# Kernel optimization log

Hardware: AMD Instinct MI355X
Metric: run time of the kernel (lower is better)

The kernel has to match this reference:

```python
import jax, jax.numpy as jnp
import numpy as np


def setup_inputs() -> dict:
    key = jax.random.key(0)
    kx, kf = jax.random.split(key)
    x = jax.random.normal(kx, (4, 8192, 1024), dtype=jnp.float32)
    filt = jax.random.normal(kf, (2048,), dtype=jnp.float32)
    return {"x": x, "filt": filt}


def reference(x, filt):
    # x: (batch, seq, dim); filt: (filter_length,)
    batch, seq, dim = x.shape
    L = filt.shape[0]
    pad = seq + L - 1
    # long-sequence FFT branch (seq > 64)
    xt = jnp.swapaxes(x, 1, 2)                 # (b, d, s)
    fx = jnp.fft.rfft(xt, n=pad, axis=-1)      # (b, d, pad//2+1) complex
    ff = jnp.fft.rfft(filt[::-1], n=pad)       # (pad//2+1,) complex
    conv = jnp.fft.irfft(fx * ff, n=pad, axis=-1)  # (b, d, pad)
    conv = conv[:, :, L - 1:L - 1 + seq]       # valid region, length seq
    return jnp.swapaxes(conv, 1, 2)            # (b, s, d)
```

## Files before the change

kernel.cpp:

```cpp
#include <hip/hip_runtime.h>

typedef unsigned short u16;
typedef unsigned int   u32;

#define BATCH 4
#define SEQ   8192
#define DIM   1024
#define FL    2048
#define TROW  10240

#define BM 512
#define BN 64
#define BK 64
#define NSTAGE 40
#define WOFF 64
#define NW   2272
#define WIN_HI 2174

typedef float  f32x4  __attribute__((ext_vector_type(4)));
typedef __bf16 bf16x8 __attribute__((ext_vector_type(8)));
typedef short  s16x8  __attribute__((ext_vector_type(8)));

typedef const __attribute__((address_space(1))) void* gas_t;
typedef __attribute__((address_space(3))) void* las_t;

__device__ __forceinline__ u16 f2bf(float f) {
  u32 u = __float_as_uint(f);
  u += 0x7fffu + ((u >> 16) & 1u);
  return (u16)(u >> 16);
}

__global__ __launch_bounds__(256) void k_transpose(const float* __restrict__ x,
                                                   u16* __restrict__ xT) {
  __shared__ __align__(16) u16 sm[64 * 66];
  const int bid = blockIdx.x;
  const int tb = bid % (TROW / 64);
  const int db = (bid / (TROW / 64)) % (DIM / 64);
  const int b  = bid / ((TROW / 64) * (DIM / 64));
  const int t0 = tb * 64, d0 = db * 64;
  const int tid = threadIdx.x;

  const int c4 = tid & 15;
  const int lt = tid >> 4;
  const float* xb = x + (size_t)b * SEQ * DIM + d0 + c4 * 4;
  #pragma unroll
  for (int s = 0; s < 64; s += 16) {
    const int tl = lt + s;
    const int t = t0 + tl;
    float4 v = make_float4(0.f, 0.f, 0.f, 0.f);
    if (t < SEQ) v = *(const float4*)(xb + (size_t)t * DIM);
    u32 p0 = (u32)f2bf(v.x) | ((u32)f2bf(v.y) << 16);
    u32 p1 = (u32)f2bf(v.z) | ((u32)f2bf(v.w) << 16);
    u32* dst = (u32*)&sm[tl * 66 + c4 * 4];
    dst[0] = p0;
    dst[1] = p1;
  }
  __syncthreads();
  const int q  = tid & 7;
  const int dl = tid >> 3;
  u16* xo = xT + ((size_t)b * DIM + d0) * TROW + t0 + 8 * q;
  #pragma unroll
  for (int s = 0; s < 2; ++s) {
    const int d = dl + 32 * s;
    u32 w[4];
    #pragma unroll
    for (int h = 0; h < 4; ++h) {
      w[h] = (u32)sm[(8 * q + 2 * h) * 66 + d] |
             ((u32)sm[(8 * q + 2 * h + 1) * 66 + d] << 16);
    }
    *(uint4*)(xo + (size_t)d * TROW) = *(const uint4*)w;
  }
}

__global__ __launch_bounds__(256, 2) void k_conv(const u16* __restrict__ xT,
                                                 const float* __restrict__ filt,
                                                 float* __restrict__ out) {
  __shared__ __align__(16) u16 Wb[NW * 8];
  __shared__ __align__(16) u16 Xs[2][BN * BK];

  const int bid = blockIdx.x;
  const int tb = bid & 15;
  const int db = (bid >> 4) & 15;
  const int b  = bid >> 8;
  const int t0 = tb * BM;
  const int d0 = db * BN;

  const int tid  = threadIdx.x;
  const int wid  = tid >> 6;
  const int lane = tid & 63;
  const int quad = lane >> 4;
  const int lq   = lane & 15;
  const int Tw   = wid * 128;

  for (int w = tid; w < NW; w += 256) {
    const int base = w - WOFF;
    u32 pk[4];
    #pragma unroll
    for (int h = 0; h < 4; ++h) {
      const int i0 = base + 2 * h;
      const int i1 = i0 + 1;
      const float v0 = (i0 >= 0 && i0 < FL) ? filt[i0] : 0.f;
      const float v1 = (i1 >= 0 && i1 < FL) ? filt[i1] : 0.f;
      pk[h] = (u32)f2bf(v0) | ((u32)f2bf(v1) << 16);
    }
    u32* dst = (u32*)&Wb[w * 8];
    dst[0] = pk[0]; dst[1] = pk[1]; dst[2] = pk[2]; dst[3] = pk[3];
  }

  const u16* xrow = xT + ((size_t)b * DIM + d0) * TROW + t0;
  const int p0 = wid * 128 + lane;
  const int p1 = p0 + 64;
  const int ds0 = p0 >> 3, kc0 = (p0 & 7) ^ (ds0 & 7);
  const int ds1 = p1 >> 3, kc1 = (p1 & 7) ^ (ds1 & 7);
  const u16* gp0 = xrow + (size_t)ds0 * TROW + kc0 * 8;
  const u16* gp1 = xrow + (size_t)ds1 * TROW + kc1 * 8;

  f32x4 acc[8][4];
  const f32x4 fz = {0.f, 0.f, 0.f, 0.f};
  #pragma unroll
  for (int i = 0; i < 8; ++i)
    #pragma unroll
    for (int j = 0; j < 4; ++j) acc[i][j] = fz;

  const s16x8 sz = {0, 0, 0, 0, 0, 0, 0, 0};
  bf16x8 roll0 = __builtin_bit_cast(bf16x8, sz);
  bf16x8 roll1 = roll0, roll2 = roll0, roll3 = roll0, roll4 = roll0, roll5 = roll0;

  const int wconst = quad * 8 - Tw - lq + WOFF;
  const int kkLo = Tw - 31;
  const int kkHi = Tw + WIN_HI;

  {
    u16* nb = &Xs[0][wid * 1024];
    __builtin_amdgcn_global_load_lds((gas_t)gp0, (las_t)nb, 16, 0, 0);
    __builtin_amdgcn_global_load_lds((gas_t)gp1, (las_t)(nb + 512), 16, 0, 0);
  }

  for (int st = 0; st < NSTAGE; ++st) {
    __syncthreads();
    if (st + 1 < NSTAGE) {
      const int kkn = (st + 1) * BK;
      u16* nb = &Xs[(st + 1) & 1][wid * 1024];
      __builtin_amdgcn_global_load_lds((gas_t)(gp0 + kkn), (las_t)nb, 16, 0, 0);
      __builtin_amdgcn_global_load_lds((gas_t)(gp1 + kkn), (las_t)(nb + 512), 16, 0, 0);
    }
    const u16* Xc = &Xs[st & 1][0];
    const int kk0 = st * BK;
    #pragma unroll
    for (int half = 0; half < 2; ++half) {
      const int kk = kk0 + half * 32;
      if (kk >= kkLo && kk <= kkHi) {
        bf16x8 bfr[4];
        #pragma unroll
        for (int nt = 0; nt < 4; ++nt) {
          const int dl = nt * 16 + lq;
          const int kc = (half * 4 + quad) ^ (dl & 7);
          bfr[nt] = *(const bf16x8*)&Xc[(dl * 8 + kc) * 8];
        }
        const int w0 = kk + wconst;
        const bf16x8 a0 = *(const bf16x8*)&Wb[w0 * 8];
        const bf16x8 a1 = *(const bf16x8*)&Wb[(w0 - 16) * 8];
        #pragma unroll
        for (int nt = 0; nt < 4; ++nt) {
          acc[0][nt] = __builtin_amdgcn_mfma_f32_16x16x32_bf16(a0,    bfr[nt], acc[0][nt], 0, 0, 0);
          acc[1][nt] = __builtin_amdgcn_mfma_f32_16x16x32_bf16(a1,    bfr[nt], acc[1][nt], 0, 0, 0);
          acc[2][nt] = __builtin_amdgcn_mfma_f32_16x16x32_bf16(roll0, bfr[nt], acc[2][nt], 0, 0, 0);
          acc[3][nt] = __builtin_amdgcn_mfma_f32_16x16x32_bf16(roll1, bfr[nt], acc[3][nt], 0, 0, 0);
          acc[4][nt] = __builtin_amdgcn_mfma_f32_16x16x32_bf16(roll2, bfr[nt], acc[4][nt], 0, 0, 0);
          acc[5][nt] = __builtin_amdgcn_mfma_f32_16x16x32_bf16(roll3, bfr[nt], acc[5][nt], 0, 0, 0);
          acc[6][nt] = __builtin_amdgcn_mfma_f32_16x16x32_bf16(roll4, bfr[nt], acc[6][nt], 0, 0, 0);
          acc[7][nt] = __builtin_amdgcn_mfma_f32_16x16x32_bf16(roll5, bfr[nt], acc[7][nt], 0, 0, 0);
        }
        roll5 = roll3; roll4 = roll2; roll3 = roll1; roll2 = roll0;
        roll1 = a1; roll0 = a0;
      }
    }
  }

  float* ob = out + ((size_t)b * SEQ + t0 + Tw) * DIM + d0;
  #pragma unroll
  for (int mt = 0; mt < 8; ++mt) {
    #pragma unroll
    for (int nt = 0; nt < 4; ++nt) {
      #pragma unroll
      for (int r = 0; r < 4; ++r) {
        ob[(size_t)(mt * 16 + quad * 4 + r) * DIM + nt * 16 + lq] = acc[mt][nt][r];
      }
    }
  }
}

extern "C" void kernel_launch(void* const* d_in, const int* in_sizes, int n_in,
                              void* d_out, int out_size, void* d_ws, size_t ws_size,
                              hipStream_t stream) {
  const float* x    = (const float*)d_in[0];
  const float* filt = (const float*)d_in[1];
  float* out = (float*)d_out;
  u16* xT = (u16*)d_ws;
  (void)in_sizes; (void)n_in; (void)out_size; (void)ws_size;

  k_transpose<<<BATCH * (TROW / 64) * (DIM / 64), 256, 0, stream>>>(x, xT);
  k_conv<<<BATCH * 16 * 16, 256, 0, stream>>>(xT, filt, out);
}
```

Baseline: 345.0 us.

## Load X fragments directly from global, drop LDS staging and skip out-of-window steps

Removes the LDS double buffer and per-stage __syncthreads for the X operand; each wave now loads its B fragments straight from global memory into registers. The loop iterates only over the wave's own valid k-window (68 half-steps), so inactive steps are no longer visited. The shifting register roll is replaced by a 4-deep ring indexed statically through an unroll-by-4. This removes barrier and LDS traffic but exposes global load latency with no software prefetch, and the four waves now re-read overlapping X data separately.

After: 372.0 us. 7.8% more time.

```diff
diff --git a/kernel.cpp b/kernel.cpp
--- a/kernel.cpp
+++ b/kernel.cpp
@@ -11,18 +11,13 @@
 
 #define BM 512
 #define BN 64
-#define BK 64
-#define NSTAGE 40
 #define WOFF 64
 #define NW   2272
-#define WIN_HI 2174
+#define NHALF 68
 
 typedef float  f32x4  __attribute__((ext_vector_type(4)));
 typedef __bf16 bf16x8 __attribute__((ext_vector_type(8)));
 typedef short  s16x8  __attribute__((ext_vector_type(8)));
-
-typedef const __attribute__((address_space(1))) void* gas_t;
-typedef __attribute__((address_space(3))) void* las_t;
 
 __device__ __forceinline__ u16 f2bf(float f) {
   u32 u = __float_as_uint(f);
@@ -76,7 +71,6 @@
                                                  const float* __restrict__ filt,
                                                  float* __restrict__ out) {
   __shared__ __align__(16) u16 Wb[NW * 8];
-  __shared__ __align__(16) u16 Xs[2][BN * BK];
 
   const int bid = blockIdx.x;
   const int tb = bid & 15;
@@ -106,14 +100,13 @@
     u32* dst = (u32*)&Wb[w * 8];
     dst[0] = pk[0]; dst[1] = pk[1]; dst[2] = pk[2]; dst[3] = pk[3];
   }
+  __syncthreads();
 
-  const u16* xrow = xT + ((size_t)b * DIM + d0) * TROW + t0;
-  const int p0 = wid * 128 + lane;
-  const int p1 = p0 + 64;
-  const int ds0 = p0 >> 3, kc0 = (p0 & 7) ^ (ds0 & 7);
-  const int ds1 = p1 >> 3, kc1 = (p1 & 7) ^ (ds1 & 7);
-  const u16* gp0 = xrow + (size_t)ds0 * TROW + kc0 * 8;
-  const u16* gp1 = xrow + (size_t)ds1 * TROW + kc1 * 8;
+  const u16* xrow = xT + ((size_t)b * DIM + d0) * TROW + t0 + quad * 8;
+  const u16* gB0 = xrow + (size_t)(0 * 16 + lq) * TROW;
+  const u16* gB1 = xrow + (size_t)(1 * 16 + lq) * TROW;
+  const u16* gB2 = xrow + (size_t)(2 * 16 + lq) * TROW;
+  const u16* gB3 = xrow + (size_t)(3 * 16 + lq) * TROW;
 
   f32x4 acc[8][4];
   const f32x4 fz = {0.f, 0.f, 0.f, 0.f};
@@ -123,56 +116,36 @@
     for (int j = 0; j < 4; ++j) acc[i][j] = fz;
 
   const s16x8 sz = {0, 0, 0, 0, 0, 0, 0, 0};
-  bf16x8 roll0 = __builtin_bit_cast(bf16x8, sz);
-  bf16x8 roll1 = roll0, roll2 = roll0, roll3 = roll0, roll4 = roll0, roll5 = roll0;
+  bf16x8 A0[4], A1[4];
+  A0[1] = A0[2] = A0[3] = __builtin_bit_cast(bf16x8, sz);
+  A1[1] = A1[2] = A1[3] = A0[1];
+  A0[0] = A0[1]; A1[0] = A1[1];
 
   const int wconst = quad * 8 - Tw - lq + WOFF;
-  const int kkLo = Tw - 31;
-  const int kkHi = Tw + WIN_HI;
+  const int kkBase = 4 * wid * 32;
 
-  {
-    u16* nb = &Xs[0][wid * 1024];
-    __builtin_amdgcn_global_load_lds((gas_t)gp0, (las_t)nb, 16, 0, 0);
-    __builtin_amdgcn_global_load_lds((gas_t)gp1, (las_t)(nb + 512), 16, 0, 0);
-  }
-
-  for (int st = 0; st < NSTAGE; ++st) {
-    __syncthreads();
-    if (st + 1 < NSTAGE) {
-      const int kkn = (st + 1) * BK;
-      u16* nb = &Xs[(st + 1) & 1][wid * 1024];
-      __builtin_amdgcn_global_load_lds((gas_t)(gp0 + kkn), (las_t)nb, 16, 0, 0);
-      __builtin_amdgcn_global_load_lds((gas_t)(gp1 + kkn), (las_t)(nb + 512), 16, 0, 0);
-    }
-    const u16* Xc = &Xs[st & 1][0];
-    const int kk0 = st * BK;
+  for (int g = 0; g < NHALF / 4; ++g) {
     #pragma unroll
-    for (int half = 0; half < 2; ++half) {
-      const int kk = kk0 + half * 32;
-      if (kk >= kkLo && kk <= kkHi) {
-        bf16x8 bfr[4];
-        #pragma unroll
-        for (int nt = 0; nt < 4; ++nt) {
-          const int dl = nt * 16 + lq;
-          const int kc = (half * 4 + quad) ^ (dl & 7);
-          bfr[nt] = *(const bf16x8*)&Xc[(dl * 8 + kc) * 8];
-        }
-        const int w0 = kk + wconst;
-        const bf16x8 a0 = *(const bf16x8*)&Wb[w0 * 8];
-        const bf16x8 a1 = *(const bf16x8*)&Wb[(w0 - 16) * 8];
-        #pragma unroll
-        for (int nt = 0; nt < 4; ++nt) {
-          acc[0][nt] = __builtin_amdgcn_mfma_f32_16x16x32_bf16(a0,    bfr[nt], acc[0][nt], 0, 0, 0);
-          acc[1][nt] = __builtin_amdgcn_mfma_f32_16x16x32_bf16(a1,    bfr[nt], acc[1][nt], 0, 0, 0);
-          acc[2][nt] = __builtin_amdgcn_mfma_f32_16x16x32_bf16(roll0, bfr[nt], acc[2][nt], 0, 0, 0);
-          acc[3][nt] = __builtin_amdgcn_mfma_f32_16x16x32_bf16(roll1, bfr[nt], acc[3][nt], 0, 0, 0);
-          acc[4][nt] = __builtin_amdgcn_mfma_f32_16x16x32_bf16(roll2, bfr[nt], acc[4][nt], 0, 0, 0);
-          acc[5][nt] = __builtin_amdgcn_mfma_f32_16x16x32_bf16(roll3, bfr[nt], acc[5][nt], 0, 0, 0);
-          acc[6][nt] = __builtin_amdgcn_mfma_f32_16x16x32_bf16(roll4, bfr[nt], acc[6][nt], 0, 0, 0);
-          acc[7][nt] = __builtin_amdgcn_mfma_f32_16x16x32_bf16(roll5, bfr[nt], acc[7][nt], 0, 0, 0);
-        }
-        roll5 = roll3; roll4 = roll2; roll3 = roll1; roll2 = roll0;
-        roll1 = a1; roll0 = a0;
+    for (int r = 0; r < 4; ++r) {
+      const int kk = kkBase + (g * 4 + r) * 32;
+      bf16x8 bfr[4];
+      bfr[0] = *(const bf16x8*)(gB0 + kk);
+      bfr[1] = *(const bf16x8*)(gB1 + kk);
+      bfr[2] = *(const bf16x8*)(gB2 + kk);
+      bfr[3] = *(const bf16x8*)(gB3 + kk);
+      const int w0 = kk + wconst;
+      A0[r] = *(const bf16x8*)&Wb[w0 * 8];
+      A1[r] = *(const bf16x8*)&Wb[(w0 - 16) * 8];
+      #pragma unroll
+      for (int nt = 0; nt < 4; ++nt) {
+        acc[0][nt] = __builtin_amdgcn_mfma_f32_16x16x32_bf16(A0[r],           bfr[nt], acc[0][nt], 0, 0, 0);
+        acc[1][nt] = __builtin_amdgcn_mfma_f32_16x16x32_bf16(A1[r],           bfr[nt], acc[1][nt], 0, 0, 0);
+        acc[2][nt] = __builtin_amdgcn_mfma_f32_16x16x32_bf16(A0[(r + 3) & 3], bfr[nt], acc[2][nt], 0, 0, 0);
+        acc[3][nt] = __builtin_amdgcn_mfma_f32_16x16x32_bf16(A1[(r + 3) & 3], bfr[nt], acc[3][nt], 0, 0, 0);
+        acc[4][nt] = __builtin_amdgcn_mfma_f32_16x16x32_bf16(A0[(r + 2) & 3], bfr[nt], acc[4][nt], 0, 0, 0);
+        acc[5][nt] = __builtin_amdgcn_mfma_f32_16x16x32_bf16(A1[(r + 2) & 3], bfr[nt], acc[5][nt], 0, 0, 0);
+        acc[6][nt] = __builtin_amdgcn_mfma_f32_16x16x32_bf16(A0[(r + 1) & 3], bfr[nt], acc[6][nt], 0, 0, 0);
+        acc[7][nt] = __builtin_amdgcn_mfma_f32_16x16x32_bf16(A1[(r + 1) & 3], bfr[nt], acc[7][nt], 0, 0, 0);
       }
     }
   }
```
